# Kernel optimization log

Hardware: AMD Instinct MI355X
Metric: run time of the kernel (lower is better)

## Reference

```python
import jax, jax.numpy as jnp
import numpy as np
import math

N, T, D, H = 8, 1024, 768, 12

def setup_inputs() -> dict:
    key = jax.random.key(0)
    ks = jax.random.split(key, 5)
    s = 1.0 / math.sqrt(D)
    return {
        "x": jax.random.normal(ks[0], (N, T, D), dtype=jnp.float32),
        "Wq": jax.random.normal(ks[1], (D, D), dtype=jnp.float32) * s,
        "Wk": jax.random.normal(ks[2], (D, D), dtype=jnp.float32) * s,
        "Wv": jax.random.normal(ks[3], (D, D), dtype=jnp.float32) * s,
        "Wo": jax.random.normal(ks[4], (D, D), dtype=jnp.float32) * s,
        "bo": jnp.zeros((D,), dtype=jnp.float32),
    }

def reference(x, Wq, Wk, Wv, Wo, bo):
    n, t, d = x.shape
    h = H
    dh = d // h  # 64
    # nn.Linear: y = x @ W.T
    q = (x @ Wq.T).reshape(n, t, h, dh).transpose(0, 2, 1, 3)  # [n,h,t,dh]
    k = (x @ Wk.T).reshape(n, t, h, dh).transpose(0, 2, 1, 3)
    v = (x @ Wv.T).reshape(n, t, h, dh).transpose(0, 2, 1, 3)
    scores = jnp.einsum('nhqd,nhkd->nhqk', q, k) / math.sqrt(dh)  # [n,h,t,t]
    causal = jnp.tril(jnp.ones((t, t), dtype=bool))
    scores = jnp.where(causal, scores, -jnp.inf)
    attn = jax.nn.softmax(scores, axis=-1)
    out = jnp.einsum('nhqk,nhkd->nhqd', attn, v)  # [n,h,t,dh]
    out = out.transpose(0, 2, 1, 3).reshape(n, t, d)
    return out @ Wo.T + bo
```

## Files before the change

kernel.cpp:

```cpp
#include <hip/hip_runtime.h>

typedef __attribute__((ext_vector_type(8))) short short8;
typedef __attribute__((ext_vector_type(4))) float f32x4;
typedef __attribute__((ext_vector_type(4))) short short4v;
typedef __attribute__((ext_vector_type(4))) unsigned short ushort4v;

#define DEV static __device__ __forceinline__

DEV unsigned short f2bf(float f) {
  unsigned int u = __builtin_bit_cast(unsigned int, f);
  u += 0x7fffu + ((u >> 16) & 1u);
  return (unsigned short)(u >> 16);
}

DEV unsigned int pack2bf(float a, float b) {
  return (unsigned int)f2bf(a) | ((unsigned int)f2bf(b) << 16);
}

DEV void gload16(const void* g, void* l) {
  __builtin_amdgcn_global_load_lds(
      (const __attribute__((address_space(1))) unsigned int*)g,
      (__attribute__((address_space(3))) unsigned int*)l, 16, 0, 0);
}

__global__ __launch_bounds__(256) void cvt_bf16(const float* __restrict__ in,
                                                unsigned short* __restrict__ out,
                                                int nvec4) {
  int i = blockIdx.x * 256 + threadIdx.x;
  if (i >= nvec4) return;
  float4 v = ((const float4*)in)[i];
  ushort4v o = {f2bf(v.x), f2bf(v.y), f2bf(v.z), f2bf(v.w)};
  *(ushort4v*)(out + (size_t)i * 4) = o;
}

__global__ __launch_bounds__(256) void cvt_w4(const float* __restrict__ w0,
                                              const float* __restrict__ w1,
                                              const float* __restrict__ w2,
                                              const float* __restrict__ w3,
                                              unsigned short* __restrict__ out) {
  int i = blockIdx.x * 256 + threadIdx.x;
  int wsel = i / 147456;
  int j = i - wsel * 147456;
  const float* src = wsel == 0 ? w0 : wsel == 1 ? w1 : wsel == 2 ? w2 : w3;
  float4 v = ((const float4*)src)[j];
  ushort4v o = {f2bf(v.x), f2bf(v.y), f2bf(v.z), f2bf(v.w)};
  *(ushort4v*)(out + (size_t)i * 4) = o;
}

__global__ __launch_bounds__(256) void gemm_qkv(const short* __restrict__ A,
                                                const short* __restrict__ B0,
                                                unsigned short* __restrict__ QK,
                                                unsigned short* __restrict__ Vt) {
  __shared__ short As[128 * 32];
  __shared__ short Bs[128 * 32];
  const int tid = threadIdx.x;
  const int lane = tid & 63;
  const int wave = tid >> 6;
  const int row0 = blockIdx.x * 128;
  const int wsel = blockIdx.y / 6;
  const int col0 = (blockIdx.y % 6) * 128;
  const short* B = B0 + (size_t)wsel * 589824;
  const int wr = (wave >> 1) * 64;
  const int wc = (wave & 1) * 64;

  f32x4 acc[4][4] = {};

  const short* aG = A + (size_t)(row0 + wave * 16 + (lane >> 2)) * 768 + (lane & 3) * 8;
  const short* bG = B + (size_t)(col0 + wave * 16 + (lane >> 2)) * 768 + (lane & 3) * 8;
  char* aL = (char*)As + wave * 1024;
  char* bL = (char*)Bs + wave * 1024;

  const int cl = lane & 15;
  const int g8 = (lane >> 4) * 8;

  for (int kk = 0; kk < 768; kk += 32) {
    gload16(aG + kk, aL);
    gload16(aG + 64 * 768 + kk, aL + 4096);
    gload16(bG + kk, bL);
    gload16(bG + 64 * 768 + kk, bL + 4096);
    __syncthreads();
    short8 af[4], bfr[4];
#pragma unroll
    for (int m = 0; m < 4; m++) af[m] = *(const short8*)&As[(wr + m * 16 + cl) * 32 + g8];
#pragma unroll
    for (int n = 0; n < 4; n++) bfr[n] = *(const short8*)&Bs[(wc + n * 16 + cl) * 32 + g8];
#pragma unroll
    for (int m = 0; m < 4; m++)
#pragma unroll
      for (int n = 0; n < 4; n++)
        acc[m][n] = __builtin_amdgcn_mfma_f32_16x16x32_bf16(af[m], bfr[n], acc[m][n], 0, 0, 0);
    __syncthreads();
  }

  const int r4 = (lane >> 4) * 4;
  unsigned short* Qout = QK + (size_t)wsel * 6291456;
#pragma unroll
  for (int m = 0; m < 4; m++) {
#pragma unroll
    for (int n = 0; n < 4; n++) {
#pragma unroll
      for (int r = 0; r < 4; r++) {
        const int row = row0 + wr + m * 16 + r4 + r;
        const int col = col0 + wc + n * 16 + cl;
        const unsigned short v = f2bf(acc[m][n][r]);
        if (wsel < 2) {
          Qout[(size_t)((((row >> 10) * 12 + (col >> 6)) << 16) +
                        ((row & 1023) << 6) + (col & 63))] = v;
        } else {
          Vt[(size_t)((((row >> 10) * 12 + (col >> 6)) << 16) +
                      ((col & 63) << 10) + (row & 1023))] = v;
        }
      }
    }
  }
}

__global__ __launch_bounds__(256) void gemm_out(const short* __restrict__ A,
                                                const short* __restrict__ B,
                                                float* __restrict__ Cout,
                                                const float* __restrict__ bias) {
  __shared__ short As[128 * 32];
  __shared__ short Bs[128 * 32];
  const int tid = threadIdx.x;
  const int lane = tid & 63;
  const int wave = tid >> 6;
  const int row0 = blockIdx.x * 128;
  const int col0 = blockIdx.y * 128;
  const int wr = (wave >> 1) * 64;
  const int wc = (wave & 1) * 64;

  f32x4 acc[4][4] = {};

  const short* aG = A + (size_t)(row0 + wave * 16 + (lane >> 2)) * 768 + (lane & 3) * 8;
  const short* bG = B + (size_t)(col0 + wave * 16 + (lane >> 2)) * 768 + (lane & 3) * 8;
  char* aL = (char*)As + wave * 1024;
  char* bL = (char*)Bs + wave * 1024;

  const int cl = lane & 15;
  const int g8 = (lane >> 4) * 8;

  for (int kk = 0; kk < 768; kk += 32) {
    gload16(aG + kk, aL);
    gload16(aG + 64 * 768 + kk, aL + 4096);
    gload16(bG + kk, bL);
    gload16(bG + 64 * 768 + kk, bL + 4096);
    __syncthreads();
    short8 af[4], bfr[4];
#pragma unroll
    for (int m = 0; m < 4; m++) af[m] = *(const short8*)&As[(wr + m * 16 + cl) * 32 + g8];
#pragma unroll
    for (int n = 0; n < 4; n++) bfr[n] = *(const short8*)&Bs[(wc + n * 16 + cl) * 32 + g8];
#pragma unroll
    for (int m = 0; m < 4; m++)
#pragma unroll
      for (int n = 0; n < 4; n++)
        acc[m][n] = __builtin_amdgcn_mfma_f32_16x16x32_bf16(af[m], bfr[n], acc[m][n], 0, 0, 0);
    __syncthreads();
  }

  const int r4 = (lane >> 4) * 4;
#pragma unroll
  for (int m = 0; m < 4; m++) {
#pragma unroll
    for (int n = 0; n < 4; n++) {
#pragma unroll
      for (int r = 0; r < 4; r++) {
        const int row = row0 + wr + m * 16 + r4 + r;
        const int col = col0 + wc + n * 16 + cl;
        Cout[(size_t)row * 768 + col] = acc[m][n][r] + bias[col];
      }
    }
  }
}

__global__ __launch_bounds__(256) void attn_fwd(const short* __restrict__ Qh,
                                                const short* __restrict__ Kh,
                                                const short* __restrict__ Vt,
                                                short* __restrict__ Obuf) {
  __shared__ short Ks[32 * 72];
  __shared__ short Vs[64 * 40];
  __shared__ unsigned int Ps[4][16 * 36];

  const int tid = threadIdx.x;
  const int lane = tid & 63;
  const int w = tid >> 6;
  const int nh = blockIdx.y;
  const int nIdx = nh / 12;
  const int hIdx = nh % 12;
  const int hb = nh << 16;
  const int qloc = lane & 15;
  const int g = lane >> 4;
  const int kRow = tid >> 3, kColB = (tid & 7) * 8;
  const int vRow = tid >> 2, vColB = (tid & 3) * 8;

  for (int rep = 0; rep < 2; rep++) {
    const int qb = rep ? (15 - blockIdx.x) : blockIdx.x;
    const int qr0 = qb * 64 + w * 16;
    const int qg = qr0 + qloc;
    const int qmax = qr0 + 15;
    const int kv_end = qb * 64 + 64;

    short8 qf[2];
    qf[0] = *(const short8*)&Qh[hb + qg * 64 + g * 8];
    qf[1] = *(const short8*)&Qh[hb + qg * 64 + 32 + g * 8];

    float m_run = -INFINITY, l_run = 0.f;
    f32x4 o[4] = {};

    for (int kv0 = 0; kv0 < kv_end; kv0 += 32) {
      *(short8*)&Ks[kRow * 72 + kColB] = *(const short8*)&Kh[hb + (kv0 + kRow) * 64 + kColB];
      *(short8*)&Vs[vRow * 40 + vColB] = *(const short8*)&Vt[hb + vRow * 1024 + kv0 + vColB];
      __syncthreads();
      if (kv0 <= qmax) {
        f32x4 s[2] = {};
#pragma unroll
        for (int c = 0; c < 2; c++) {
          short8 a0 = *(const short8*)&Ks[qloc * 72 + c * 32 + g * 8];
          short8 a1 = *(const short8*)&Ks[(16 + qloc) * 72 + c * 32 + g * 8];
          s[0] = __builtin_amdgcn_mfma_f32_16x16x32_bf16(a0, qf[c], s[0], 0, 0, 0);
          s[1] = __builtin_amdgcn_mfma_f32_16x16x32_bf16(a1, qf[c], s[1], 0, 0, 0);
        }
        float pv[2][4];
        float pm = -INFINITY;
#pragma unroll
        for (int kt = 0; kt < 2; kt++)
#pragma unroll
          for (int r = 0; r < 4; r++) {
            const int kg = kv0 + kt * 16 + g * 4 + r;
            float sv = s[kt][r] * 0.125f;
            sv = (kg <= qg) ? sv : -INFINITY;
            pv[kt][r] = sv;
            pm = fmaxf(pm, sv);
          }
        pm = fmaxf(pm, __shfl_xor(pm, 16));
        pm = fmaxf(pm, __shfl_xor(pm, 32));
        const float mnew = fmaxf(m_run, pm);
        const float corr = __expf(m_run - mnew);
        float lsum = 0.f;
#pragma unroll
        for (int kt = 0; kt < 2; kt++)
#pragma unroll
          for (int r = 0; r < 4; r++) {
            float p = __expf(pv[kt][r] - mnew);
            pv[kt][r] = p;
            lsum += p;
          }
        lsum += __shfl_xor(lsum, 16);
        lsum += __shfl_xor(lsum, 32);
        l_run = l_run * corr + lsum;
        m_run = mnew;
#pragma unroll
        for (int dt = 0; dt < 4; dt++) o[dt] *= corr;
        unsigned int* pr = &Ps[w][qloc * 36];
#pragma unroll
        for (int kt = 0; kt < 2; kt++) {
          pr[kt * 8 + g * 2] = pack2bf(pv[kt][0], pv[kt][1]);
          pr[kt * 8 + g * 2 + 1] = pack2bf(pv[kt][2], pv[kt][3]);
        }
        __asm__ volatile("" ::: "memory");
        short8 pf = *(const short8*)((const short*)&Ps[w][0] + qloc * 72 + g * 8);
#pragma unroll
        for (int dt = 0; dt < 4; dt++) {
          short8 vf = *(const short8*)&Vs[(dt * 16 + qloc) * 40 + g * 8];
          o[dt] = __builtin_amdgcn_mfma_f32_16x16x32_bf16(vf, pf, o[dt], 0, 0, 0);
        }
      }
      __syncthreads();
    }

    const float inv = 1.f / l_run;
    const int outRow = nIdx * 1024 + qr0 + qloc;
    short* op = Obuf + (size_t)outRow * 768 + hIdx * 64;
#pragma unroll
    for (int dt = 0; dt < 4; dt++) {
      short4v ov;
#pragma unroll
      for (int r = 0; r < 4; r++) ov[r] = (short)f2bf(o[dt][r] * inv);
      *(short4v*)(op + dt * 16 + g * 4) = ov;
    }
  }
}

extern "C" void kernel_launch(void* const* d_in, const int* in_sizes, int n_in,
                              void* d_out, int out_size, void* d_ws, size_t ws_size,
                              hipStream_t stream) {
  (void)in_sizes; (void)n_in; (void)out_size; (void)ws_size;
  const float* x  = (const float*)d_in[0];
  const float* Wq = (const float*)d_in[1];
  const float* Wk = (const float*)d_in[2];
  const float* Wv = (const float*)d_in[3];
  const float* Wo = (const float*)d_in[4];
  const float* bo = (const float*)d_in[5];

  char* ws = (char*)d_ws;
  short* xb  = (short*)(ws);
  short* wqb = (short*)(ws + 12582912);
  short* wob = (short*)(ws + 12582912 + 3 * 1179648);
  short* Qh  = (short*)(ws + 17301504);
  short* Kh  = (short*)(ws + 17301504 + 12582912);
  short* Vt  = (short*)(ws + 17301504 + 2 * 12582912);
  short* Ob  = (short*)(ws + 17301504 + 3 * 12582912);

  cvt_bf16<<<6144, 256, 0, stream>>>(x, (unsigned short*)xb, 1572864);
  cvt_w4<<<2304, 256, 0, stream>>>(Wq, Wk, Wv, Wo, (unsigned short*)wqb);

  gemm_qkv<<<dim3(64, 18), 256, 0, stream>>>(xb, wqb, (unsigned short*)Qh,
                                             (unsigned short*)Vt);

  attn_fwd<<<dim3(8, 96), 256, 0, stream>>>(Qh, Kh, Vt, Ob);

  gemm_out<<<dim3(64, 6), 256, 0, stream>>>(Ob, wob, (float*)d_out, bo);
}
```

Baseline: 225.9 us.

## Double-buffer LDS tiles in QKV and output GEMMs, vectorize V transpose stores

```diff
diff --git a/kernel.cpp b/kernel.cpp
--- a/kernel.cpp
+++ b/kernel.cpp
@@ -51,8 +51,8 @@
                                                 const short* __restrict__ B0,
                                                 unsigned short* __restrict__ QK,
                                                 unsigned short* __restrict__ Vt) {
-  __shared__ short As[128 * 32];
-  __shared__ short Bs[128 * 32];
+  __shared__ short As[2][128 * 32];
+  __shared__ short Bs[2][128 * 32];
   const int tid = threadIdx.x;
   const int lane = tid & 63;
   const int wave = tid >> 6;
@@ -67,30 +67,43 @@
 
   const short* aG = A + (size_t)(row0 + wave * 16 + (lane >> 2)) * 768 + (lane & 3) * 8;
   const short* bG = B + (size_t)(col0 + wave * 16 + (lane >> 2)) * 768 + (lane & 3) * 8;
-  char* aL = (char*)As + wave * 1024;
-  char* bL = (char*)Bs + wave * 1024;
+  char* aL = (char*)&As[0][0] + wave * 1024;
+  char* bL = (char*)&Bs[0][0] + wave * 1024;
 
   const int cl = lane & 15;
   const int g8 = (lane >> 4) * 8;
 
-  for (int kk = 0; kk < 768; kk += 32) {
-    gload16(aG + kk, aL);
-    gload16(aG + 64 * 768 + kk, aL + 4096);
-    gload16(bG + kk, bL);
-    gload16(bG + 64 * 768 + kk, bL + 4096);
+#define QKV_STAGE(buf, kk)                          \
+  do {                                              \
+    gload16(aG + (kk), aL + (buf)*8192);            \
+    gload16(aG + 64 * 768 + (kk), aL + (buf)*8192 + 4096); \
+    gload16(bG + (kk), bL + (buf)*8192);            \
+    gload16(bG + 64 * 768 + (kk), bL + (buf)*8192 + 4096); \
+  } while (0)
+
+#define QKV_COMPUTE(buf)                                                          \
+  do {                                                                            \
+    short8 af[4], bfr[4];                                                         \
+    _Pragma("unroll") for (int m = 0; m < 4; m++)                                 \
+        af[m] = *(const short8*)&As[buf][(wr + m * 16 + cl) * 32 + g8];           \
+    _Pragma("unroll") for (int n = 0; n < 4; n++)                                 \
+        bfr[n] = *(const short8*)&Bs[buf][(wc + n * 16 + cl) * 32 + g8];          \
+    _Pragma("unroll") for (int m = 0; m < 4; m++)                                 \
+        _Pragma("unroll") for (int n = 0; n < 4; n++)                             \
+            acc[m][n] = __builtin_amdgcn_mfma_f32_16x16x32_bf16(af[m], bfr[n],    \
+                                                                acc[m][n], 0, 0, 0); \
+  } while (0)
+
+  QKV_STAGE(0, 0);
+  __syncthreads();
+  int cur = 0;
+  for (int kk = 32; kk < 768; kk += 32) {
+    QKV_STAGE(cur ^ 1, kk);
+    QKV_COMPUTE(cur);
     __syncthreads();
-    short8 af[4], bfr[4];
-#pragma unroll
-    for (int m = 0; m < 4; m++) af[m] = *(const short8*)&As[(wr + m * 16 + cl) * 32 + g8];
-#pragma unroll
-    for (int n = 0; n < 4; n++) bfr[n] = *(const short8*)&Bs[(wc + n * 16 + cl) * 32 + g8];
-#pragma unroll
-    for (int m = 0; m < 4; m++)
-#pragma unroll
-      for (int n = 0; n < 4; n++)
-        acc[m][n] = __builtin_amdgcn_mfma_f32_16x16x32_bf16(af[m], bfr[n], acc[m][n], 0, 0, 0);
-    __syncthreads();
-  }
+    cur ^= 1;
+  }
+  QKV_COMPUTE(cur);
 
   const int r4 = (lane >> 4) * 4;
   unsigned short* Qout = QK + (size_t)wsel * 6291456;
@@ -98,18 +111,20 @@
   for (int m = 0; m < 4; m++) {
 #pragma unroll
     for (int n = 0; n < 4; n++) {
-#pragma unroll
-      for (int r = 0; r < 4; r++) {
-        const int row = row0 + wr + m * 16 + r4 + r;
-        const int col = col0 + wc + n * 16 + cl;
-        const unsigned short v = f2bf(acc[m][n][r]);
-        if (wsel < 2) {
-          Qout[(size_t)((((row >> 10) * 12 + (col >> 6)) << 16) +
-                        ((row & 1023) << 6) + (col & 63))] = v;
-        } else {
-          Vt[(size_t)((((row >> 10) * 12 + (col >> 6)) << 16) +
-                      ((col & 63) << 10) + (row & 1023))] = v;
+      const int row = row0 + wr + m * 16 + r4;
+      const int col = col0 + wc + n * 16 + cl;
+      if (wsel < 2) {
+#pragma unroll
+        for (int r = 0; r < 4; r++) {
+          Qout[(size_t)(((((row + r) >> 10) * 12 + (col >> 6)) << 16) +
+                        (((row + r) & 1023) << 6) + (col & 63))] = f2bf(acc[m][n][r]);
         }
+      } else {
+        short4v ov;
+#pragma unroll
+        for (int r = 0; r < 4; r++) ov[r] = (short)f2bf(acc[m][n][r]);
+        *(short4v*)((short*)Vt + (size_t)((((row >> 10) * 12 + (col >> 6)) << 16) +
+                                          ((col & 63) << 10) + (row & 1023))) = ov;
       }
     }
   }
@@ -119,8 +134,8 @@
                                                 const short* __restrict__ B,
                                                 float* __restrict__ Cout,
                                                 const float* __restrict__ bias) {
-  __shared__ short As[128 * 32];
-  __shared__ short Bs[128 * 32];
+  __shared__ short As[2][128 * 32];
+  __shared__ short Bs[2][128 * 32];
   const int tid = threadIdx.x;
   const int lane = tid & 63;
   const int wave = tid >> 6;
@@ -133,30 +148,22 @@
 
   const short* aG = A + (size_t)(row0 + wave * 16 + (lane >> 2)) * 768 + (lane & 3) * 8;
   const short* bG = B + (size_t)(col0 + wave * 16 + (lane >> 2)) * 768 + (lane & 3) * 8;
-  char* aL = (char*)As + wave * 1024;
-  char* bL = (char*)Bs + wave * 1024;
+  char* aL = (char*)&As[0][0] + wave * 1024;
+  char* bL = (char*)&Bs[0][0] + wave * 1024;
 
   const int cl = lane & 15;
   const int g8 = (lane >> 4) * 8;
 
-  for (int kk = 0; kk < 768; kk += 32) {
-    gload16(aG + kk, aL);
-    gload16(aG + 64 * 768 + kk, aL + 4096);
-    gload16(bG + kk, bL);
-    gload16(bG + 64 * 768 + kk, bL + 4096);
+  QKV_STAGE(0, 0);
+  __syncthreads();
+  int cur = 0;
+  for (int kk = 32; kk < 768; kk += 32) {
+    QKV_STAGE(cur ^ 1, kk);
+    QKV_COMPUTE(cur);
     __syncthreads();
-    short8 af[4], bfr[4];
-#pragma unroll
-    for (int m = 0; m < 4; m++) af[m] = *(const short8*)&As[(wr + m * 16 + cl) * 32 + g8];
-#pragma unroll
-    for (int n = 0; n < 4; n++) bfr[n] = *(const short8*)&Bs[(wc + n * 16 + cl) * 32 + g8];
-#pragma unroll
-    for (int m = 0; m < 4; m++)
-#pragma unroll
-      for (int n = 0; n < 4; n++)
-        acc[m][n] = __builtin_amdgcn_mfma_f32_16x16x32_bf16(af[m], bfr[n], acc[m][n], 0, 0, 0);
-    __syncthreads();
-  }
+    cur ^= 1;
+  }
+  QKV_COMPUTE(cur);
 
   const int r4 = (lane >> 4) * 4;
 #pragma unroll
```

New measurement: 204.8 us. 9.3% less time.
